# Kernel optimization log

Hardware: AMD Instinct MI355X
Metric: run time of the kernel (lower is better)

Reference implementation:

```python
import jax, jax.numpy as jnp
import numpy as np

WEIGHT_SCALE = 0.01      # weight_scale buffer
WEIGHT_ZP = 8            # weight_zero_point buffer
BIAS_SCALE = 0.01 * 0.047  # bias_scale = weight_scale * activation_scale (from_float)
OUT_FEATURES = 4096
IN_FEATURES = 4096


def setup_inputs() -> dict:
    key = jax.random.key(0)
    k1, k2, k3 = jax.random.split(key, 3)
    x = jax.random.normal(k1, (8, 2048, IN_FEATURES), dtype=jnp.float32)
    # packed uint8 bytes, two 4-bit weights per byte; stored as int32 (values 0..255)
    packed_weight = jax.random.randint(k2, (OUT_FEATURES, IN_FEATURES // 2), 0, 256, dtype=jnp.int32)
    quantized_bias = jax.random.randint(k3, (OUT_FEATURES,), -500, 500, dtype=jnp.int32)
    return {"x": x, "packed_weight": packed_weight, "quantized_bias": quantized_bias}


def _dequantize_weights(packed_weight):
    # low nibble -> even input column, high nibble -> odd input column
    low = packed_weight & 15          # [O, I/2]
    high = (packed_weight >> 4) & 15  # [O, I/2]
    q = jnp.stack([low, high], axis=-1).reshape(OUT_FEATURES, IN_FEATURES)
    return WEIGHT_SCALE * (q.astype(jnp.float32) - WEIGHT_ZP)


def reference(x, packed_weight, quantized_bias):
    W = _dequantize_weights(packed_weight)                 # [O, I]
    b = BIAS_SCALE * quantized_bias.astype(jnp.float32)    # [O]
    # F.linear: x @ W.T + b
    return jnp.einsum('bsi,oi->bso', x, W) + b
```

## Files before the change

### kernel.cpp

```cpp
#include <hip/hip_runtime.h>


typedef __bf16 bf16x8 __attribute__((ext_vector_type(8)));
typedef float f32x4 __attribute__((ext_vector_type(4)));
typedef unsigned short u16;
typedef u16 u16x4 __attribute__((ext_vector_type(4)));
typedef u16 u16x8 __attribute__((ext_vector_type(8)));

static constexpr int Kdim = 4096;
static constexpr int Ndim = 4096;
static constexpr int BM = 256, BN = 256, BK = 64;
static constexpr int NKT = Kdim / BK;
static constexpr int TBUF = BM * BK;

__device__ __forceinline__ u16 f2bf(float f) {
  union { float f; unsigned u; } c; c.f = f;
  unsigned u = c.u;
  return (u16)((u + 0x7FFFu + ((u >> 16) & 1u)) >> 16);
}

__global__ __launch_bounds__(256) void cvt_x_kernel(const float* __restrict__ x,
                                                    u16* __restrict__ xb, int n4) {
  int stride = gridDim.x * blockDim.x;
  for (int i = blockIdx.x * blockDim.x + threadIdx.x; i < n4; i += stride) {
    float4 v = reinterpret_cast<const float4*>(x)[i];
    u16x4 o;
    o.x = f2bf(v.x); o.y = f2bf(v.y); o.z = f2bf(v.z); o.w = f2bf(v.w);
    reinterpret_cast<u16x4*>(xb)[i] = o;
  }
}

__global__ __launch_bounds__(256) void dequant_w_kernel(const int* __restrict__ pw,
                                                        u16* __restrict__ wb, int n4) {
  int stride = gridDim.x * blockDim.x;
  for (int i = blockIdx.x * blockDim.x + threadIdx.x; i < n4; i += stride) {
    int4 v = reinterpret_cast<const int4*>(pw)[i];
    int a[4] = {v.x, v.y, v.z, v.w};
    u16x8 o;
#pragma unroll
    for (int j = 0; j < 4; ++j) {
      o[2 * j]     = f2bf((float)((a[j] & 15) - 8));
      o[2 * j + 1] = f2bf((float)(((a[j] >> 4) & 15) - 8));
    }
    reinterpret_cast<u16x8*>(wb)[i] = o;
  }
}

__device__ __forceinline__ void gload16(const u16* g, const u16* l) {
  __builtin_amdgcn_global_load_lds(
      (const __attribute__((address_space(1))) void*)g,
      (__attribute__((address_space(3))) void*)l,
      16, 0, 0);
}

__global__ __launch_bounds__(512, 2) void gemm_kernel(const u16* __restrict__ A,
                                                      const u16* __restrict__ B,
                                                      const int* __restrict__ qbias,
                                                      float* __restrict__ C,
                                                      int Ntiles) {
  extern __shared__ u16 smem[];
  u16* As = smem;
  u16* Bs = smem + 3 * TBUF;

  const int tid = threadIdx.x;
  const int lane = tid & 63;
  const int wave = tid >> 6;
  const int wm = wave >> 2, wn = wave & 3;

  const int cpx = gridDim.x >> 3;
  const int bid = blockIdx.x;
  const int swz = (bid & 7) * cpx + (bid >> 3);
  const int bx = swz % Ntiles;
  const int by = swz / Ntiles;
  const int m0 = by * BM, n0 = bx * BN;

  const int srow = tid >> 3;
  const int fcol = (((tid & 7) ^ (srow & 7)) << 3);
  const u16* pa[4];
  const u16* pb[4];
#pragma unroll
  for (int i = 0; i < 4; ++i) {
    pa[i] = A + (size_t)(m0 + i * 64 + srow) * Kdim + fcol;
    pb[i] = B + (size_t)(n0 + i * 64 + srow) * Kdim + fcol;
  }
  const int wbase = (tid & 0x1C0) * 8;

  const int e0 = ((lane >> 4) ^ (lane & 7)) << 3;
  const int e1 = e0 ^ 32;
  const int arow = (wm * 128 + (lane & 15)) * 64;
  const int brow = (wn * 64 + (lane & 15)) * 64;

  f32x4 acc[8][4] = {};

#pragma unroll
  for (int i = 0; i < 4; ++i) gload16(pb[i], Bs + i * 4096 + wbase);
#pragma unroll
  for (int i = 0; i < 4; ++i) gload16(pa[i], As + i * 4096 + wbase);
#pragma unroll
  for (int i = 0; i < 4; ++i) gload16(pa[i] + BK, As + TBUF + i * 4096 + wbase);
  asm volatile("s_waitcnt vmcnt(4)" ::: "memory");
  __builtin_amdgcn_s_barrier();

  int rbuf = 0;
  for (int t = 0; t < NKT; ++t) {
    const u16* aL = As + rbuf * TBUF;
    const u16* bL = Bs + (t & 1) * TBUF;
    const u16* aW = As + ((rbuf + 2) % 3) * TBUF;
    const u16* bW = Bs + ((t + 1) & 1) * TBUF;
    const bool stb = (t + 1) < NKT;
    const bool sta = (t + 2) < NKT;
    const int kob = (t + 1) * BK;
    const int koa = (t + 2) * BK;

    bf16x8 a0[4], a1[4], bf[4][2];

#pragma unroll
    for (int m = 0; m < 4; ++m)
      a0[m] = *(const bf16x8*)(aL + arow + m * 1024 + e0);
#pragma unroll
    for (int n = 0; n < 4; ++n)
      bf[n][0] = *(const bf16x8*)(bL + brow + n * 1024 + e0);
#pragma unroll
    for (int n = 0; n < 4; ++n)
      bf[n][1] = *(const bf16x8*)(bL + brow + n * 1024 + e1);

#pragma unroll
    for (int m = 0; m < 4; ++m)
      a1[m] = *(const bf16x8*)(aL + arow + 4096 + m * 1024 + e0);
    if (stb) { gload16(pb[0] + kob, bW + 0 * 4096 + wbase);
               gload16(pb[1] + kob, bW + 1 * 4096 + wbase); }
    asm volatile("s_waitcnt lgkmcnt(4)" ::: "memory");
    __builtin_amdgcn_sched_barrier(0);
    __builtin_amdgcn_s_setprio(1);
#pragma unroll
    for (int m = 0; m < 4; ++m)
#pragma unroll
      for (int n = 0; n < 4; ++n)
        acc[m][n] = __builtin_amdgcn_mfma_f32_16x16x32_bf16(a0[m], bf[n][0], acc[m][n], 0, 0, 0);
    __builtin_amdgcn_s_setprio(0);

#pragma unroll
    for (int m = 0; m < 4; ++m)
      a0[m] = *(const bf16x8*)(aL + arow + m * 1024 + e1);
    if (stb) { gload16(pb[2] + kob, bW + 2 * 4096 + wbase);
               gload16(pb[3] + kob, bW + 3 * 4096 + wbase); }
    asm volatile("s_waitcnt lgkmcnt(4)" ::: "memory");
    __builtin_amdgcn_sched_barrier(0);
    __builtin_amdgcn_s_setprio(1);
#pragma unroll
    for (int m = 0; m < 4; ++m)
#pragma unroll
      for (int n = 0; n < 4; ++n)
        acc[4 + m][n] = __builtin_amdgcn_mfma_f32_16x16x32_bf16(a1[m], bf[n][0], acc[4 + m][n], 0, 0, 0);
    __builtin_amdgcn_s_setprio(0);

#pragma unroll
    for (int m = 0; m < 4; ++m)
      a1[m] = *(const bf16x8*)(aL + arow + 4096 + m * 1024 + e1);
    if (sta) { gload16(pa[0] + koa, aW + 0 * 4096 + wbase);
               gload16(pa[1] + koa, aW + 1 * 4096 + wbase); }
    asm volatile("s_waitcnt lgkmcnt(4)" ::: "memory");
    __builtin_amdgcn_sched_barrier(0);
    __builtin_amdgcn_s_setprio(1);
#pragma unroll
    for (int m = 0; m < 4; ++m)
#pragma unroll
      for (int n = 0; n < 4; ++n)
        acc[m][n] = __builtin_amdgcn_mfma_f32_16x16x32_bf16(a0[m], bf[n][1], acc[m][n], 0, 0, 0);
    __builtin_amdgcn_s_setprio(0);

    if (sta) { gload16(pa[2] + koa, aW + 2 * 4096 + wbase);
               gload16(pa[3] + koa, aW + 3 * 4096 + wbase); }
    asm volatile("s_waitcnt lgkmcnt(0)" ::: "memory");
    __builtin_amdgcn_sched_barrier(0);
    __builtin_amdgcn_s_setprio(1);
#pragma unroll
    for (int m = 0; m < 4; ++m)
#pragma unroll
      for (int n = 0; n < 4; ++n)
        acc[4 + m][n] = __builtin_amdgcn_mfma_f32_16x16x32_bf16(a1[m], bf[n][1], acc[4 + m][n], 0, 0, 0);
    __builtin_amdgcn_s_setprio(0);
    __builtin_amdgcn_sched_barrier(0);

    if (sta)      asm volatile("s_waitcnt vmcnt(4)" ::: "memory");
    else if (stb) asm volatile("s_waitcnt vmcnt(0)" ::: "memory");
    __builtin_amdgcn_s_barrier();

    rbuf = (rbuf == 2) ? 0 : rbuf + 1;
  }

  const float wscale = 0.01f;
  const float bscale = (float)(0.01 * 0.047);
  const int col0 = n0 + wn * 64 + (lane & 15);
  const int row0 = m0 + wm * 128 + ((lane >> 4) << 2);
#pragma unroll
  for (int n = 0; n < 4; ++n) {
    const int col = col0 + n * 16;
    const float bias = bscale * (float)qbias[col];
#pragma unroll
    for (int m = 0; m < 8; ++m) {
      const int rr = row0 + m * 16;
#pragma unroll
      for (int j = 0; j < 4; ++j)
        C[(size_t)(rr + j) * Ndim + col] = wscale * acc[m][n][j] + bias;
    }
  }
}

extern "C" void kernel_launch(void* const* d_in, const int* in_sizes, int n_in,
                              void* d_out, int out_size, void* d_ws, size_t ws_size,
                              hipStream_t stream) {
  const float* x  = (const float*)d_in[0];
  const int*   pw = (const int*)d_in[1];
  const int*   qb = (const int*)d_in[2];
  float* out = (float*)d_out;

  const int M = in_sizes[0] / Kdim;

  u16* xb = (u16*)d_ws;
  u16* wb = (u16*)((char*)d_ws + (size_t)M * Kdim * 2);

  cvt_x_kernel<<<2048, 256, 0, stream>>>(x, xb, M * Kdim / 4);
  dequant_w_kernel<<<1024, 256, 0, stream>>>(pw, wb, Ndim * Kdim / 8);

  const int Ntiles = Ndim / BN;
  const int nwg = (M / BM) * Ntiles;
  static const size_t lds_bytes = 5u * TBUF * sizeof(u16);
  (void)hipFuncSetAttribute((const void*)gemm_kernel,
                            hipFuncAttributeMaxDynamicSharedMemorySize,
                            (int)lds_bytes);
  gemm_kernel<<<nwg, 512, lds_bytes, stream>>>(xb, wb, qb, out, Ntiles);
}
```

Measured before the change: 539.6 us.

## Fuse fp32-to-bf16 activation conversion into GEMM A-tile loading

Removes the separate x conversion kernel. The GEMM now loads fp32 activations into registers, converts them to bf16, and writes them into LDS. The A buffering goes from triple to double to fit the register-staged path, with explicit vmcnt/lgkmcnt waits interleaved between MFMA groups. This avoids writing and re-reading a 128MB bf16 copy of x, but each A tile is now read at fp32 width by every N-tile workgroup and costs VGPRs and conversion ALU work.

Result: slower. 736.8 us (+36.6%).

```diff
diff --git a/kernel.cpp b/kernel.cpp
--- a/kernel.cpp
+++ b/kernel.cpp
@@ -4,7 +4,6 @@
 typedef __bf16 bf16x8 __attribute__((ext_vector_type(8)));
 typedef float f32x4 __attribute__((ext_vector_type(4)));
 typedef unsigned short u16;
-typedef u16 u16x4 __attribute__((ext_vector_type(4)));
 typedef u16 u16x8 __attribute__((ext_vector_type(8)));
 
 static constexpr int Kdim = 4096;
@@ -17,17 +16,6 @@
   union { float f; unsigned u; } c; c.f = f;
   unsigned u = c.u;
   return (u16)((u + 0x7FFFu + ((u >> 16) & 1u)) >> 16);
-}
-
-__global__ __launch_bounds__(256) void cvt_x_kernel(const float* __restrict__ x,
-                                                    u16* __restrict__ xb, int n4) {
-  int stride = gridDim.x * blockDim.x;
-  for (int i = blockIdx.x * blockDim.x + threadIdx.x; i < n4; i += stride) {
-    float4 v = reinterpret_cast<const float4*>(x)[i];
-    u16x4 o;
-    o.x = f2bf(v.x); o.y = f2bf(v.y); o.z = f2bf(v.z); o.w = f2bf(v.w);
-    reinterpret_cast<u16x4*>(xb)[i] = o;
-  }
 }
 
 __global__ __launch_bounds__(256) void dequant_w_kernel(const int* __restrict__ pw,
@@ -53,14 +41,21 @@
       16, 0, 0);
 }
 
-__global__ __launch_bounds__(512, 2) void gemm_kernel(const u16* __restrict__ A,
+__device__ __forceinline__ bf16x8 cvt8(float4 lo, float4 hi) {
+  bf16x8 v;
+  v[0] = (__bf16)lo.x; v[1] = (__bf16)lo.y; v[2] = (__bf16)lo.z; v[3] = (__bf16)lo.w;
+  v[4] = (__bf16)hi.x; v[5] = (__bf16)hi.y; v[6] = (__bf16)hi.z; v[7] = (__bf16)hi.w;
+  return v;
+}
+
+__global__ __launch_bounds__(512, 2) void gemm_kernel(const float* __restrict__ A32,
                                                       const u16* __restrict__ B,
                                                       const int* __restrict__ qbias,
                                                       float* __restrict__ C,
                                                       int Ntiles) {
   extern __shared__ u16 smem[];
   u16* As = smem;
-  u16* Bs = smem + 3 * TBUF;
+  u16* Bs = smem + 2 * TBUF;
 
   const int tid = threadIdx.x;
   const int lane = tid & 63;
@@ -76,14 +71,15 @@
 
   const int srow = tid >> 3;
   const int fcol = (((tid & 7) ^ (srow & 7)) << 3);
-  const u16* pa[4];
   const u16* pb[4];
+  const float* pa32[4];
 #pragma unroll
   for (int i = 0; i < 4; ++i) {
-    pa[i] = A + (size_t)(m0 + i * 64 + srow) * Kdim + fcol;
-    pb[i] = B + (size_t)(n0 + i * 64 + srow) * Kdim + fcol;
+    pb[i]   = B   + (size_t)(n0 + i * 64 + srow) * Kdim + fcol;
+    pa32[i] = A32 + (size_t)(m0 + i * 64 + srow) * Kdim + fcol;
   }
   const int wbase = (tid & 0x1C0) * 8;
+  const int dstA = tid * 8;
 
   const int e0 = ((lane >> 4) ^ (lane & 7)) << 3;
   const int e1 = e0 ^ 32;
@@ -91,26 +87,39 @@
   const int brow = (wn * 64 + (lane & 15)) * 64;
 
   f32x4 acc[8][4] = {};
-
+  float4 st[8];
+
+#pragma unroll
+  for (int i = 0; i < 4; ++i) {
+    st[2 * i]     = *(const float4*)(pa32[i]);
+    st[2 * i + 1] = *(const float4*)(pa32[i] + 4);
+  }
 #pragma unroll
   for (int i = 0; i < 4; ++i) gload16(pb[i], Bs + i * 4096 + wbase);
-#pragma unroll
-  for (int i = 0; i < 4; ++i) gload16(pa[i], As + i * 4096 + wbase);
-#pragma unroll
-  for (int i = 0; i < 4; ++i) gload16(pa[i] + BK, As + TBUF + i * 4096 + wbase);
   asm volatile("s_waitcnt vmcnt(4)" ::: "memory");
+#pragma unroll
+  for (int i = 0; i < 4; ++i)
+    *(bf16x8*)(As + i * 4096 + dstA) = cvt8(st[2 * i], st[2 * i + 1]);
+  asm volatile("s_waitcnt vmcnt(0) lgkmcnt(0)" ::: "memory");
   __builtin_amdgcn_s_barrier();
 
-  int rbuf = 0;
-  for (int t = 0; t < NKT; ++t) {
-    const u16* aL = As + rbuf * TBUF;
+#define MFMAS(ACC_BASE, AF, KH)                                               \
+    __builtin_amdgcn_sched_barrier(0);                                        \
+    __builtin_amdgcn_s_setprio(1);                                            \
+    _Pragma("unroll")                                                         \
+    for (int m = 0; m < 4; ++m)                                               \
+      _Pragma("unroll")                                                       \
+      for (int n = 0; n < 4; ++n)                                             \
+        acc[(ACC_BASE) + m][n] = __builtin_amdgcn_mfma_f32_16x16x32_bf16(     \
+            AF[m], bf[n][KH], acc[(ACC_BASE) + m][n], 0, 0, 0);               \
+    __builtin_amdgcn_s_setprio(0);
+
+  for (int t = 0; t < NKT - 1; ++t) {
+    const u16* aL = As + (t & 1) * TBUF;
     const u16* bL = Bs + (t & 1) * TBUF;
-    const u16* aW = As + ((rbuf + 2) % 3) * TBUF;
+    u16* aW = As + ((t + 1) & 1) * TBUF;
     const u16* bW = Bs + ((t + 1) & 1) * TBUF;
-    const bool stb = (t + 1) < NKT;
-    const bool sta = (t + 2) < NKT;
-    const int kob = (t + 1) * BK;
-    const int koa = (t + 2) * BK;
+    const int ko = (t + 1) * BK;
 
     bf16x8 a0[4], a1[4], bf[4][2];
 
@@ -127,67 +136,79 @@
 #pragma unroll
     for (int m = 0; m < 4; ++m)
       a1[m] = *(const bf16x8*)(aL + arow + 4096 + m * 1024 + e0);
-    if (stb) { gload16(pb[0] + kob, bW + 0 * 4096 + wbase);
-               gload16(pb[1] + kob, bW + 1 * 4096 + wbase); }
-    asm volatile("s_waitcnt lgkmcnt(4)" ::: "memory");
+    st[0] = *(const float4*)(pa32[0] + ko);
+    st[1] = *(const float4*)(pa32[0] + ko + 4);
+    st[2] = *(const float4*)(pa32[1] + ko);
+    st[3] = *(const float4*)(pa32[1] + ko + 4);
+    gload16(pb[0] + ko, bW + 0 * 4096 + wbase);
+    gload16(pb[1] + ko, bW + 1 * 4096 + wbase);
+    asm volatile("s_waitcnt lgkmcnt(4)" ::: "memory");
+    MFMAS(0, a0, 0)
+
+#pragma unroll
+    for (int m = 0; m < 4; ++m)
+      a0[m] = *(const bf16x8*)(aL + arow + m * 1024 + e1);
+    st[4] = *(const float4*)(pa32[2] + ko);
+    st[5] = *(const float4*)(pa32[2] + ko + 4);
+    st[6] = *(const float4*)(pa32[3] + ko);
+    st[7] = *(const float4*)(pa32[3] + ko + 4);
+    gload16(pb[2] + ko, bW + 2 * 4096 + wbase);
+    gload16(pb[3] + ko, bW + 3 * 4096 + wbase);
+    asm volatile("s_waitcnt lgkmcnt(4)" ::: "memory");
+    MFMAS(4, a1, 0)
+
+#pragma unroll
+    for (int m = 0; m < 4; ++m)
+      a1[m] = *(const bf16x8*)(aL + arow + 4096 + m * 1024 + e1);
+    asm volatile("s_waitcnt vmcnt(8)" ::: "memory");
+    *(bf16x8*)(aW + 0 * 4096 + dstA) = cvt8(st[0], st[1]);
+    *(bf16x8*)(aW + 1 * 4096 + dstA) = cvt8(st[2], st[3]);
+    asm volatile("s_waitcnt lgkmcnt(6)" ::: "memory");
+    MFMAS(0, a0, 1)
+
+    asm volatile("s_waitcnt vmcnt(2)" ::: "memory");
+    *(bf16x8*)(aW + 2 * 4096 + dstA) = cvt8(st[4], st[5]);
+    *(bf16x8*)(aW + 3 * 4096 + dstA) = cvt8(st[6], st[7]);
+    asm volatile("s_waitcnt lgkmcnt(4)" ::: "memory");
+    MFMAS(4, a1, 1)
     __builtin_amdgcn_sched_barrier(0);
-    __builtin_amdgcn_s_setprio(1);
-#pragma unroll
-    for (int m = 0; m < 4; ++m)
-#pragma unroll
-      for (int n = 0; n < 4; ++n)
-        acc[m][n] = __builtin_amdgcn_mfma_f32_16x16x32_bf16(a0[m], bf[n][0], acc[m][n], 0, 0, 0);
-    __builtin_amdgcn_s_setprio(0);
-
+    asm volatile("s_waitcnt vmcnt(0) lgkmcnt(0)" ::: "memory");
+    __builtin_amdgcn_s_barrier();
+  }
+
+  {
+    const int t = NKT - 1;
+    const u16* aL = As + (t & 1) * TBUF;
+    const u16* bL = Bs + (t & 1) * TBUF;
+    bf16x8 a0[4], a1[4], bf[4][2];
+#pragma unroll
+    for (int m = 0; m < 4; ++m)
+      a0[m] = *(const bf16x8*)(aL + arow + m * 1024 + e0);
+#pragma unroll
+    for (int n = 0; n < 4; ++n)
+      bf[n][0] = *(const bf16x8*)(bL + brow + n * 1024 + e0);
+#pragma unroll
+    for (int n = 0; n < 4; ++n)
+      bf[n][1] = *(const bf16x8*)(bL + brow + n * 1024 + e1);
+#pragma unroll
+    for (int m = 0; m < 4; ++m)
+      a1[m] = *(const bf16x8*)(aL + arow + 4096 + m * 1024 + e0);
+    asm volatile("s_waitcnt lgkmcnt(4)" ::: "memory");
+    MFMAS(0, a0, 0)
 #pragma unroll
     for (int m = 0; m < 4; ++m)
       a0[m] = *(const bf16x8*)(aL + arow + m * 1024 + e1);
-    if (stb) { gload16(pb[2] + kob, bW + 2 * 4096 + wbase);
-               gload16(pb[3] + kob, bW + 3 * 4096 + wbase); }
-    asm volatile("s_waitcnt lgkmcnt(4)" ::: "memory");
-    __builtin_amdgcn_sched_barrier(0);
-    __builtin_amdgcn_s_setprio(1);
-#pragma unroll
-    for (int m = 0; m < 4; ++m)
-#pragma unroll
-      for (int n = 0; n < 4; ++n)
-        acc[4 + m][n] = __builtin_amdgcn_mfma_f32_16x16x32_bf16(a1[m], bf[n][0], acc[4 + m][n], 0, 0, 0);
-    __builtin_amdgcn_s_setprio(0);
-
+    asm volatile("s_waitcnt lgkmcnt(4)" ::: "memory");
+    MFMAS(4, a1, 0)
 #pragma unroll
     for (int m = 0; m < 4; ++m)
       a1[m] = *(const bf16x8*)(aL + arow + 4096 + m * 1024 + e1);
-    if (sta) { gload16(pa[0] + koa, aW + 0 * 4096 + wbase);
-               gload16(pa[1] + koa, aW + 1 * 4096 + wbase); }
-    asm volatile("s_waitcnt lgkmcnt(4)" ::: "memory");
-    __builtin_amdgcn_sched_barrier(0);
-    __builtin_amdgcn_s_setprio(1);
-#pragma unroll
-    for (int m = 0; m < 4; ++m)
-#pragma unroll
-      for (int n = 0; n < 4; ++n)
-        acc[m][n] = __builtin_amdgcn_mfma_f32_16x16x32_bf16(a0[m], bf[n][1], acc[m][n], 0, 0, 0);
-    __builtin_amdgcn_s_setprio(0);
-
-    if (sta) { gload16(pa[2] + koa, aW + 2 * 4096 + wbase);
-               gload16(pa[3] + koa, aW + 3 * 4096 + wbase); }
+    asm volatile("s_waitcnt lgkmcnt(4)" ::: "memory");
+    MFMAS(0, a0, 1)
     asm volatile("s_waitcnt lgkmcnt(0)" ::: "memory");
-    __builtin_amdgcn_sched_barrier(0);
-    __builtin_amdgcn_s_setprio(1);
-#pragma unroll
-    for (int m = 0; m < 4; ++m)
-#pragma unroll
-      for (int n = 0; n < 4; ++n)
-        acc[4 + m][n] = __builtin_amdgcn_mfma_f32_16x16x32_bf16(a1[m], bf[n][1], acc[4 + m][n], 0, 0, 0);
-    __builtin_amdgcn_s_setprio(0);
-    __builtin_amdgcn_sched_barrier(0);
-
-    if (sta)      asm volatile("s_waitcnt vmcnt(4)" ::: "memory");
-    else if (stb) asm volatile("s_waitcnt vmcnt(0)" ::: "memory");
-    __builtin_amdgcn_s_barrier();
-
-    rbuf = (rbuf == 2) ? 0 : rbuf + 1;
-  }
+    MFMAS(4, a1, 1)
+  }
+#undef MFMAS
 
   const float wscale = 0.01f;
   const float bscale = (float)(0.01 * 0.047);
@@ -217,17 +238,15 @@
 
   const int M = in_sizes[0] / Kdim;
 
-  u16* xb = (u16*)d_ws;
-  u16* wb = (u16*)((char*)d_ws + (size_t)M * Kdim * 2);
-
-  cvt_x_kernel<<<2048, 256, 0, stream>>>(x, xb, M * Kdim / 4);
+  u16* wb = (u16*)d_ws;
+
   dequant_w_kernel<<<1024, 256, 0, stream>>>(pw, wb, Ndim * Kdim / 8);
 
   const int Ntiles = Ndim / BN;
   const int nwg = (M / BM) * Ntiles;
-  static const size_t lds_bytes = 5u * TBUF * sizeof(u16);
+  static const size_t lds_bytes = 4u * TBUF * sizeof(u16);
   (void)hipFuncSetAttribute((const void*)gemm_kernel,
                             hipFuncAttributeMaxDynamicSharedMemorySize,
                             (int)lds_bytes);
-  gemm_kernel<<<nwg, 512, lds_bytes, stream>>>(xb, wb, qb, out, Ntiles);
-}
+  gemm_kernel<<<nwg, 512, lds_bytes, stream>>>(x, wb, qb, out, Ntiles);
+}
```
